# Kernel tuning notes

Hardware: AMD Instinct MI355X
Metric: run time of the kernel (lower is better)

The kernel has to match this reference:

```python
import jax, jax.numpy as jnp
import numpy as np

D_MODEL = 1024
N_HEADS = 16
FEATURE_DIM = 16
HEAD_DIM = D_MODEL // N_HEADS  # 64
EPS = 1e-12


def taylor_exp(x):
    """2nd-order Taylor feature map of exp(q^T k / sqrt(d)).
    x: (b, h, l, d) -> (b, h, l, 1 + d + d^2)"""
    d = x.shape[-1]
    rd = jnp.sqrt(jnp.asarray(d, x.dtype))      # sqrt(d)
    rrd = jnp.sqrt(rd)                          # d^(1/4)
    r2 = jnp.sqrt(jnp.asarray(2.0, x.dtype))
    x2 = (x[..., :, None] * x[..., None, :]).reshape(*x.shape[:-1], d * d) / r2
    ones = jnp.ones_like(x[..., :1])
    return jnp.concatenate([ones, x / rrd, x2 / rd], axis=-1)


def setup_inputs() -> dict:
    key = jax.random.key(0)
    k0, k1, k2, k3, k4 = jax.random.split(key, 5)
    b, l = 1, 1024
    scale = 1.0 / np.sqrt(D_MODEL)
    hidden_states = jax.random.normal(k0, (b, l, D_MODEL), dtype=jnp.float32)
    Wq = jax.random.normal(k1, (N_HEADS * FEATURE_DIM, D_MODEL), dtype=jnp.float32) * scale
    Wk = jax.random.normal(k2, (N_HEADS * FEATURE_DIM, D_MODEL), dtype=jnp.float32) * scale
    Wv = jax.random.normal(k3, (N_HEADS * HEAD_DIM, D_MODEL), dtype=jnp.float32) * scale
    Wo = jax.random.normal(k4, (D_MODEL, N_HEADS * HEAD_DIM), dtype=jnp.float32) * scale
    return {"hidden_states": hidden_states, "Wq": Wq, "Wk": Wk, "Wv": Wv, "Wo": Wo}


def reference(hidden_states, Wq, Wk, Wv, Wo):
    b, l, _ = hidden_states.shape
    # projections (bias-free)
    q = (hidden_states @ Wq.T).reshape(b, l, N_HEADS, FEATURE_DIM).transpose(0, 2, 1, 3)
    k = (hidden_states @ Wk.T).reshape(b, l, N_HEADS, FEATURE_DIM).transpose(0, 2, 1, 3)
    v = (hidden_states @ Wv.T).reshape(b, l, N_HEADS, HEAD_DIM).transpose(0, 2, 1, 3)
    qf = taylor_exp(q)   # (b, h, l, D) with D = 1 + d + d^2 = 273
    kf = taylor_exp(k)
    # causal linear attention via associative KV accumulation
    # kv_state[l] = sum_{t<=l} phi(k_t) outer v_t  -> (b, h, l, head_dim, D)
    kv_state = jnp.cumsum(kf[..., None, :] * v[..., :, None], axis=2)
    num = jnp.einsum('bhlD,bhldD->bhld', qf, kv_state)
    den = jnp.einsum('bhlD,bhlD->bhl', qf, jnp.cumsum(kf, axis=2))[..., None] + EPS
    y = num / den                                # (b, h, l, head_dim)
    y = y.transpose(0, 2, 1, 3).reshape(b, l, N_HEADS * HEAD_DIM)
    return y @ Wo.T
```

## Files before the change

### kernel.cpp

```cpp
#include <hip/hip_runtime.h>

#define LSEQ 1024
#define DMODEL 1024
#define NHEADS 16
#define FDIM 16
#define HDIM 64
#define CHUNK 64
#define NCHUNK 16

typedef __attribute__((ext_vector_type(8))) short short8;
typedef __attribute__((ext_vector_type(4))) float floatx4;

__device__ __forceinline__ float bf2f(unsigned short u) {
    unsigned int x = ((unsigned int)u) << 16;
    return __builtin_bit_cast(float, x);
}
__device__ __forceinline__ unsigned short f2bf(float f) {
    unsigned int x = __builtin_bit_cast(unsigned int, f);
    unsigned int r = (x + 0x7fffu + ((x >> 16) & 1u)) >> 16;
    return (unsigned short)r;
}

__device__ __forceinline__ int block_detect_fp32(const unsigned short* wq) {
    __shared__ int cnt;
    if (threadIdx.x == 0) cnt = 0;
    __syncthreads();
    int bad = 0;
    for (int i = threadIdx.x; i < 1024; i += blockDim.x) {
        int e = (wq[i] >> 7) & 0xFF;
        if (e >= 143 || (e > 0 && e <= 80)) bad++;
    }
    if (bad) atomicAdd(&cnt, bad);
    __syncthreads();
    return cnt > 128;
}

#define U_QB   0
#define U_KB   262144
#define U_VB   524288
#define U_YB   1572864

#define MFMA(a, b, c) __builtin_amdgcn_mfma_f32_16x16x32_bf16((a), (b), (c), 0, 0, 0)

__global__ __launch_bounds__(256) void qkv_gemm(
    const void* __restrict__ hidR, const void* __restrict__ WqR,
    const void* __restrict__ WkR, const void* __restrict__ WvR,
    unsigned short* __restrict__ qb, unsigned short* __restrict__ kb,
    unsigned short* __restrict__ vb) {
    int fp32 = block_detect_fp32((const unsigned short*)WqR);
    __shared__ __align__(16) unsigned short As[64][136];
    __shared__ __align__(16) unsigned short Bs[64][136];
    int nb = blockIdx.x, mb = blockIdx.y;
    const void* Braw; unsigned short* Cout; int ldc, col0, br0;
    if (nb < 4)      { Braw = WqR; br0 = nb * 64;       Cout = qb; ldc = 256;  col0 = nb * 64; }
    else if (nb < 8) { Braw = WkR; br0 = (nb - 4) * 64; Cout = kb; ldc = 256;  col0 = (nb - 4) * 64; }
    else             { Braw = WvR; br0 = (nb - 8) * 64; Cout = vb; ldc = 1024; col0 = (nb - 8) * 64; }

    int t = threadIdx.x;
    int r = t >> 2, c0 = (t & 3) * 32;
    int wave = t >> 6, lane = t & 63;
    int ml = lane & 15, q4 = lane >> 4;
    int mq = (wave >> 1) * 32, nq = (wave & 1) * 32;
    floatx4 acc00 = {0.f,0.f,0.f,0.f}, acc01 = acc00, acc10 = acc00, acc11 = acc00;

    for (int k0 = 0; k0 < DMODEL; k0 += 128) {
        short8 av[4], bv[4];
        if (!fp32) {
            const unsigned short* Ap = (const unsigned short*)hidR + (size_t)(mb * 64 + r) * DMODEL + k0 + c0;
            const unsigned short* Bp = (const unsigned short*)Braw + (size_t)(br0 + r) * DMODEL + k0 + c0;
            #pragma unroll
            for (int j = 0; j < 4; ++j) {
                av[j] = *(const short8*)(Ap + j * 8);
                bv[j] = *(const short8*)(Bp + j * 8);
            }
        } else {
            const float* Ap = (const float*)hidR + (size_t)(mb * 64 + r) * DMODEL + k0 + c0;
            const float* Bp = (const float*)Braw + (size_t)(br0 + r) * DMODEL + k0 + c0;
            #pragma unroll
            for (int j = 0; j < 4; ++j) {
                #pragma unroll
                for (int u = 0; u < 8; ++u) {
                    av[j][u] = (short)f2bf(Ap[j * 8 + u]);
                    bv[j][u] = (short)f2bf(Bp[j * 8 + u]);
                }
            }
        }
        __syncthreads();
        #pragma unroll
        for (int j = 0; j < 4; ++j) {
            *(short8*)&As[r][c0 + j * 8] = av[j];
            *(short8*)&Bs[r][c0 + j * 8] = bv[j];
        }
        __syncthreads();
        #pragma unroll
        for (int kk = 0; kk < 4; ++kk) {
            short8 a0 = *(const short8*)&As[mq + ml][kk * 32 + q4 * 8];
            short8 a1 = *(const short8*)&As[mq + 16 + ml][kk * 32 + q4 * 8];
            short8 b0 = *(const short8*)&Bs[nq + ml][kk * 32 + q4 * 8];
            short8 b1 = *(const short8*)&Bs[nq + 16 + ml][kk * 32 + q4 * 8];
            acc00 = MFMA(a0, b0, acc00); acc01 = MFMA(a0, b1, acc01);
            acc10 = MFMA(a1, b0, acc10); acc11 = MFMA(a1, b1, acc11);
        }
    }
    #pragma unroll
    for (int mi = 0; mi < 2; ++mi) {
        #pragma unroll
        for (int ni = 0; ni < 2; ++ni) {
            floatx4 acc = mi == 0 ? (ni == 0 ? acc00 : acc01) : (ni == 0 ? acc10 : acc11);
            int nloc = nq + ni * 16 + ml;
            #pragma unroll
            for (int r4 = 0; r4 < 4; ++r4) {
                int row = mb * 64 + mq + mi * 16 + q4 * 4 + r4;
                Cout[(size_t)row * ldc + col0 + nloc] = f2bf(acc[r4]);
            }
        }
    }
}

__global__ __launch_bounds__(256) void flash_attn(
    const unsigned short* __restrict__ qb, const unsigned short* __restrict__ kb,
    const unsigned short* __restrict__ vb, unsigned short* __restrict__ ybB) {
    int h = blockIdx.x & 15, c = blockIdx.x >> 4;
    int l0 = c * CHUNK;
    __shared__ __align__(16) unsigned short qs[64][40];
    __shared__ __align__(16) unsigned short ksm[64][40];
    __shared__ __align__(16) unsigned short vT[80][72];
    __shared__ __align__(16) unsigned short P[64][72];
    int t = threadIdx.x, lane = t & 63, wave = t >> 6;
    int ml = lane & 15, q4 = lane >> 4;
    int m0 = wave * 16;

    {
        int m = t >> 2, i4 = (t & 3) * 4;
        *(ushort4*)&qs[m][i4] = *(const ushort4*)&qb[(size_t)(l0 + m) * 256 + h * 16 + i4];
        ushort4 z = {0, 0, 0, 0};
        *(ushort4*)&qs[m][16 + i4]  = z;
        *(ushort4*)&ksm[m][16 + i4] = z;
    }
    if (t < 64) {
        vT[64][t] = 0x3F80;
        #pragma unroll
        for (int i = 65; i < 80; ++i) vT[i][t] = 0;
    }

    floatx4 acc[5];
    #pragma unroll
    for (int i = 0; i < 5; ++i) acc[i] = (floatx4){0.f, 0.f, 0.f, 0.f};

    for (int j = 0; j <= c; ++j) {
        {
            int m = t >> 2, i4 = (t & 3) * 4;
            *(ushort4*)&ksm[m][i4] = *(const ushort4*)&kb[(size_t)(j * 64 + m) * 256 + h * 16 + i4];
            int cc = (t & 3) * 16;
            unsigned short tmp[16];
            #pragma unroll
            for (int u = 0; u < 4; ++u)
                *(ushort4*)&tmp[u * 4] = *(const ushort4*)&vb[(size_t)(j * 64 + m) * 1024 + h * 64 + cc + u * 4];
            #pragma unroll
            for (int u = 0; u < 16; ++u) vT[cc + u][m] = tmp[u];
        }
        __syncthreads();

        short8 aq = *(const short8*)&qs[m0 + ml][q4 * 8];
        bool diag = (j == c);
        #pragma unroll
        for (int nt = 0; nt < 4; ++nt) {
            short8 bk = *(const short8*)&ksm[nt * 16 + ml][q4 * 8];
            floatx4 s4 = {0.f, 0.f, 0.f, 0.f};
            s4 = MFMA(aq, bk, s4);
            int tt = nt * 16 + ml;
            #pragma unroll
            for (int r = 0; r < 4; ++r) {
                int lrow = m0 + q4 * 4 + r;
                float s = s4[r];
                float p = 1.f + 0.25f * s + 0.03125f * s * s;
                if (diag && tt > lrow) p = 0.f;
                P[lrow][tt] = f2bf(p);
            }
        }

        #pragma unroll
        for (int k0 = 0; k0 < 64; k0 += 32) {
            short8 ap = *(const short8*)&P[m0 + ml][k0 + q4 * 8];
            #pragma unroll
            for (int nt = 0; nt < 5; ++nt) {
                short8 bv = *(const short8*)&vT[nt * 16 + ml][k0 + q4 * 8];
                acc[nt] = MFMA(ap, bv, acc[nt]);
            }
        }
        __syncthreads();
    }

    #pragma unroll
    for (int r = 0; r < 4; ++r) {
        float den = __shfl(acc[4][r], q4 * 16) + 1e-12f;
        float dinv = 1.f / den;
        int lrow = m0 + q4 * 4 + r;
        unsigned short* yp = ybB + (size_t)(l0 + lrow) * 1024 + h * 64;
        #pragma unroll
        for (int nt = 0; nt < 4; ++nt)
            yp[nt * 16 + ml] = f2bf(acc[nt][r] * dinv);
    }
}

__global__ __launch_bounds__(256) void out_gemm(
    const unsigned short* __restrict__ A, const void* __restrict__ WoR,
    void* __restrict__ outv, const unsigned short* __restrict__ wqraw) {
    int fp32 = block_detect_fp32(wqraw);
    __shared__ __align__(16) unsigned short As[64][136];
    __shared__ __align__(16) unsigned short Bs[64][136];
    int nb = blockIdx.x, mb = blockIdx.y;
    int br0 = nb * 64;

    int t = threadIdx.x;
    int r = t >> 2, c0 = (t & 3) * 32;
    int wave = t >> 6, lane = t & 63;
    int ml = lane & 15, q4 = lane >> 4;
    int mq = (wave >> 1) * 32, nq = (wave & 1) * 32;
    floatx4 acc00 = {0.f,0.f,0.f,0.f}, acc01 = acc00, acc10 = acc00, acc11 = acc00;

    for (int k0 = 0; k0 < DMODEL; k0 += 128) {
        short8 av[4], bv[4];
        const unsigned short* Ap = A + (size_t)(mb * 64 + r) * DMODEL + k0 + c0;
        #pragma unroll
        for (int j = 0; j < 4; ++j) av[j] = *(const short8*)(Ap + j * 8);
        if (!fp32) {
            const unsigned short* Bp = (const unsigned short*)WoR + (size_t)(br0 + r) * DMODEL + k0 + c0;
            #pragma unroll
            for (int j = 0; j < 4; ++j) bv[j] = *(const short8*)(Bp + j * 8);
        } else {
            const float* Bp = (const float*)WoR + (size_t)(br0 + r) * DMODEL + k0 + c0;
            #pragma unroll
            for (int j = 0; j < 4; ++j) {
                #pragma unroll
                for (int u = 0; u < 8; ++u) bv[j][u] = (short)f2bf(Bp[j * 8 + u]);
            }
        }
        __syncthreads();
        #pragma unroll
        for (int j = 0; j < 4; ++j) {
            *(short8*)&As[r][c0 + j * 8] = av[j];
            *(short8*)&Bs[r][c0 + j * 8] = bv[j];
        }
        __syncthreads();
        #pragma unroll
        for (int kk = 0; kk < 4; ++kk) {
            short8 a0 = *(const short8*)&As[mq + ml][kk * 32 + q4 * 8];
            short8 a1 = *(const short8*)&As[mq + 16 + ml][kk * 32 + q4 * 8];
            short8 b0 = *(const short8*)&Bs[nq + ml][kk * 32 + q4 * 8];
            short8 b1 = *(const short8*)&Bs[nq + 16 + ml][kk * 32 + q4 * 8];
            acc00 = MFMA(a0, b0, acc00); acc01 = MFMA(a0, b1, acc01);
            acc10 = MFMA(a1, b0, acc10); acc11 = MFMA(a1, b1, acc11);
        }
    }
    #pragma unroll
    for (int mi = 0; mi < 2; ++mi) {
        #pragma unroll
        for (int ni = 0; ni < 2; ++ni) {
            floatx4 acc = mi == 0 ? (ni == 0 ? acc00 : acc01) : (ni == 0 ? acc10 : acc11);
            int n = nb * 64 + nq + ni * 16 + ml;
            #pragma unroll
            for (int r4 = 0; r4 < 4; ++r4) {
                int row = mb * 64 + mq + mi * 16 + q4 * 4 + r4;
                size_t idx = (size_t)row * 1024 + n;
                if (fp32) ((float*)outv)[idx] = acc[r4];
                else      ((unsigned short*)outv)[idx] = f2bf(acc[r4]);
            }
        }
    }
}

extern "C" void kernel_launch(void* const* d_in, const int* in_sizes, int n_in,
                              void* d_out, int out_size, void* d_ws, size_t ws_size,
                              hipStream_t stream) {
    unsigned short* us = (unsigned short*)d_ws;
    unsigned short* qbB = us + U_QB;
    unsigned short* kbB = us + U_KB;
    unsigned short* vbB = us + U_VB;
    unsigned short* ybB = us + U_YB;
    size_t need = (size_t)(U_YB + 1048576) * 2ull;
    if (ws_size < need) return;

    qkv_gemm<<<dim3(24, 16), 256, 0, stream>>>(d_in[0], d_in[1], d_in[2], d_in[3], qbB, kbB, vbB);
    flash_attn<<<dim3(256), 256, 0, stream>>>(qbB, kbB, vbB, ybB);
    out_gemm<<<dim3(16, 16), 256, 0, stream>>>(ybB, d_in[4], d_out, (const unsigned short*)d_in[1]);
}
```

Baseline: 152.3 us.

## Fuse QKV GEMM, attention, and output GEMM into one cooperative persistent kernel

Replaces three kernel launches with a single cooperative kernel of 256 blocks that runs the QKV projection (384 tiles over a grid-stride loop), the chunked causal attention, and the output projection, separated by grid-wide syncs. It also adds register double-buffering of the next K-slice in the GEMM body so global loads overlap with MFMA work. This removes launch gaps and repeated fp32 detection, but the QKV stage now takes two waves of tiles on 256 blocks. The grid syncs and the unbalanced causal attention stage make every block wait for the slowest one.

```diff
diff --git a/kernel.cpp b/kernel.cpp
--- a/kernel.cpp
+++ b/kernel.cpp
@@ -1,4 +1,7 @@
 #include <hip/hip_runtime.h>
+#include <hip/hip_cooperative_groups.h>
+
+namespace cg = cooperative_groups;
 
 #define LSEQ 1024
 #define DMODEL 1024
@@ -21,20 +24,6 @@
     return (unsigned short)r;
 }
 
-__device__ __forceinline__ int block_detect_fp32(const unsigned short* wq) {
-    __shared__ int cnt;
-    if (threadIdx.x == 0) cnt = 0;
-    __syncthreads();
-    int bad = 0;
-    for (int i = threadIdx.x; i < 1024; i += blockDim.x) {
-        int e = (wq[i] >> 7) & 0xFF;
-        if (e >= 143 || (e > 0 && e <= 80)) bad++;
-    }
-    if (bad) atomicAdd(&cnt, bad);
-    __syncthreads();
-    return cnt > 128;
-}
-
 #define U_QB   0
 #define U_KB   262144
 #define U_VB   524288
@@ -42,231 +31,232 @@
 
 #define MFMA(a, b, c) __builtin_amdgcn_mfma_f32_16x16x32_bf16((a), (b), (c), 0, 0, 0)
 
-__global__ __launch_bounds__(256) void qkv_gemm(
-    const void* __restrict__ hidR, const void* __restrict__ WqR,
-    const void* __restrict__ WkR, const void* __restrict__ WvR,
-    unsigned short* __restrict__ qb, unsigned short* __restrict__ kb,
-    unsigned short* __restrict__ vb) {
-    int fp32 = block_detect_fp32((const unsigned short*)WqR);
-    __shared__ __align__(16) unsigned short As[64][136];
-    __shared__ __align__(16) unsigned short Bs[64][136];
-    int nb = blockIdx.x, mb = blockIdx.y;
-    const void* Braw; unsigned short* Cout; int ldc, col0, br0;
-    if (nb < 4)      { Braw = WqR; br0 = nb * 64;       Cout = qb; ldc = 256;  col0 = nb * 64; }
-    else if (nb < 8) { Braw = WkR; br0 = (nb - 4) * 64; Cout = kb; ldc = 256;  col0 = (nb - 4) * 64; }
-    else             { Braw = WvR; br0 = (nb - 8) * 64; Cout = vb; ldc = 1024; col0 = (nb - 8) * 64; }
-
+struct SMemGemm { unsigned short As[64][136]; unsigned short Bs[64][136]; };
+struct SMemFA {
+    unsigned short qs[64][40];
+    unsigned short ksm[64][40];
+    unsigned short vT[80][72];
+    unsigned short P[64][72];
+};
+union SMemU { SMemGemm g; SMemFA f; };
+
+__device__ __forceinline__ void gemm64_body(
+    SMemGemm& s, const void* Araw, int a_fp32, int arow0,
+    const void* Braw, int b_fp32, int brow0, floatx4 acc[4]) {
     int t = threadIdx.x;
     int r = t >> 2, c0 = (t & 3) * 32;
     int wave = t >> 6, lane = t & 63;
     int ml = lane & 15, q4 = lane >> 4;
     int mq = (wave >> 1) * 32, nq = (wave & 1) * 32;
-    floatx4 acc00 = {0.f,0.f,0.f,0.f}, acc01 = acc00, acc10 = acc00, acc11 = acc00;
-
+    #pragma unroll
+    for (int i = 0; i < 4; ++i) acc[i] = (floatx4){0.f, 0.f, 0.f, 0.f};
+
+    short8 av[4], bv[4], av2[4], bv2[4];
+    auto stage = [&](int k0, short8* a, short8* b) {
+        if (!a_fp32) {
+            const unsigned short* Ap = (const unsigned short*)Araw + (size_t)(arow0 + r) * DMODEL + k0 + c0;
+            #pragma unroll
+            for (int j = 0; j < 4; ++j) a[j] = *(const short8*)(Ap + j * 8);
+        } else {
+            const float* Ap = (const float*)Araw + (size_t)(arow0 + r) * DMODEL + k0 + c0;
+            #pragma unroll
+            for (int j = 0; j < 4; ++j)
+                #pragma unroll
+                for (int u = 0; u < 8; ++u) a[j][u] = (short)f2bf(Ap[j * 8 + u]);
+        }
+        if (!b_fp32) {
+            const unsigned short* Bp = (const unsigned short*)Braw + (size_t)(brow0 + r) * DMODEL + k0 + c0;
+            #pragma unroll
+            for (int j = 0; j < 4; ++j) b[j] = *(const short8*)(Bp + j * 8);
+        } else {
+            const float* Bp = (const float*)Braw + (size_t)(brow0 + r) * DMODEL + k0 + c0;
+            #pragma unroll
+            for (int j = 0; j < 4; ++j)
+                #pragma unroll
+                for (int u = 0; u < 8; ++u) b[j][u] = (short)f2bf(Bp[j * 8 + u]);
+        }
+    };
+
+    stage(0, av, bv);
     for (int k0 = 0; k0 < DMODEL; k0 += 128) {
-        short8 av[4], bv[4];
-        if (!fp32) {
-            const unsigned short* Ap = (const unsigned short*)hidR + (size_t)(mb * 64 + r) * DMODEL + k0 + c0;
-            const unsigned short* Bp = (const unsigned short*)Braw + (size_t)(br0 + r) * DMODEL + k0 + c0;
-            #pragma unroll
-            for (int j = 0; j < 4; ++j) {
-                av[j] = *(const short8*)(Ap + j * 8);
-                bv[j] = *(const short8*)(Bp + j * 8);
-            }
-        } else {
-            const float* Ap = (const float*)hidR + (size_t)(mb * 64 + r) * DMODEL + k0 + c0;
-            const float* Bp = (const float*)Braw + (size_t)(br0 + r) * DMODEL + k0 + c0;
-            #pragma unroll
-            for (int j = 0; j < 4; ++j) {
-                #pragma unroll
-                for (int u = 0; u < 8; ++u) {
-                    av[j][u] = (short)f2bf(Ap[j * 8 + u]);
-                    bv[j][u] = (short)f2bf(Bp[j * 8 + u]);
-                }
-            }
-        }
         __syncthreads();
         #pragma unroll
         for (int j = 0; j < 4; ++j) {
-            *(short8*)&As[r][c0 + j * 8] = av[j];
-            *(short8*)&Bs[r][c0 + j * 8] = bv[j];
-        }
-        __syncthreads();
+            *(short8*)&s.As[r][c0 + j * 8] = av[j];
+            *(short8*)&s.Bs[r][c0 + j * 8] = bv[j];
+        }
+        __syncthreads();
+        if (k0 + 128 < DMODEL) stage(k0 + 128, av2, bv2);
         #pragma unroll
         for (int kk = 0; kk < 4; ++kk) {
-            short8 a0 = *(const short8*)&As[mq + ml][kk * 32 + q4 * 8];
-            short8 a1 = *(const short8*)&As[mq + 16 + ml][kk * 32 + q4 * 8];
-            short8 b0 = *(const short8*)&Bs[nq + ml][kk * 32 + q4 * 8];
-            short8 b1 = *(const short8*)&Bs[nq + 16 + ml][kk * 32 + q4 * 8];
-            acc00 = MFMA(a0, b0, acc00); acc01 = MFMA(a0, b1, acc01);
-            acc10 = MFMA(a1, b0, acc10); acc11 = MFMA(a1, b1, acc11);
-        }
-    }
-    #pragma unroll
-    for (int mi = 0; mi < 2; ++mi) {
-        #pragma unroll
-        for (int ni = 0; ni < 2; ++ni) {
-            floatx4 acc = mi == 0 ? (ni == 0 ? acc00 : acc01) : (ni == 0 ? acc10 : acc11);
-            int nloc = nq + ni * 16 + ml;
-            #pragma unroll
-            for (int r4 = 0; r4 < 4; ++r4) {
-                int row = mb * 64 + mq + mi * 16 + q4 * 4 + r4;
-                Cout[(size_t)row * ldc + col0 + nloc] = f2bf(acc[r4]);
-            }
-        }
-    }
-}
-
-__global__ __launch_bounds__(256) void flash_attn(
-    const unsigned short* __restrict__ qb, const unsigned short* __restrict__ kb,
-    const unsigned short* __restrict__ vb, unsigned short* __restrict__ ybB) {
-    int h = blockIdx.x & 15, c = blockIdx.x >> 4;
-    int l0 = c * CHUNK;
-    __shared__ __align__(16) unsigned short qs[64][40];
-    __shared__ __align__(16) unsigned short ksm[64][40];
-    __shared__ __align__(16) unsigned short vT[80][72];
-    __shared__ __align__(16) unsigned short P[64][72];
+            short8 a0 = *(const short8*)&s.As[mq + ml][kk * 32 + q4 * 8];
+            short8 a1 = *(const short8*)&s.As[mq + 16 + ml][kk * 32 + q4 * 8];
+            short8 b0 = *(const short8*)&s.Bs[nq + ml][kk * 32 + q4 * 8];
+            short8 b1 = *(const short8*)&s.Bs[nq + 16 + ml][kk * 32 + q4 * 8];
+            acc[0] = MFMA(a0, b0, acc[0]); acc[1] = MFMA(a0, b1, acc[1]);
+            acc[2] = MFMA(a1, b0, acc[2]); acc[3] = MFMA(a1, b1, acc[3]);
+        }
+        #pragma unroll
+        for (int j = 0; j < 4; ++j) { av[j] = av2[j]; bv[j] = bv2[j]; }
+    }
+    __syncthreads();
+}
+
+__global__ __launch_bounds__(256) void mega(
+    const void* __restrict__ hidR, const void* __restrict__ WqR,
+    const void* __restrict__ WkR, const void* __restrict__ WvR,
+    const void* __restrict__ WoR, void* __restrict__ outv,
+    unsigned short* __restrict__ qb, unsigned short* __restrict__ kb,
+    unsigned short* __restrict__ vb, unsigned short* __restrict__ ybB) {
+    cg::grid_group grid = cg::this_grid();
+    __shared__ __align__(16) SMemU sm;
+    int bid = blockIdx.x;
     int t = threadIdx.x, lane = t & 63, wave = t >> 6;
     int ml = lane & 15, q4 = lane >> 4;
-    int m0 = wave * 16;
-
+
+    int fp32;
     {
-        int m = t >> 2, i4 = (t & 3) * 4;
-        *(ushort4*)&qs[m][i4] = *(const ushort4*)&qb[(size_t)(l0 + m) * 256 + h * 16 + i4];
-        ushort4 z = {0, 0, 0, 0};
-        *(ushort4*)&qs[m][16 + i4]  = z;
-        *(ushort4*)&ksm[m][16 + i4] = z;
-    }
-    if (t < 64) {
-        vT[64][t] = 0x3F80;
-        #pragma unroll
-        for (int i = 65; i < 80; ++i) vT[i][t] = 0;
-    }
-
-    floatx4 acc[5];
-    #pragma unroll
-    for (int i = 0; i < 5; ++i) acc[i] = (floatx4){0.f, 0.f, 0.f, 0.f};
-
-    for (int j = 0; j <= c; ++j) {
+        __shared__ int cnt;
+        if (t == 0) cnt = 0;
+        __syncthreads();
+        const unsigned short* wq = (const unsigned short*)WqR;
+        int bad = 0;
+        for (int i = t; i < 1024; i += 256) {
+            int e = (wq[i] >> 7) & 0xFF;
+            if (e >= 143 || (e > 0 && e <= 80)) bad++;
+        }
+        if (bad) atomicAdd(&cnt, bad);
+        __syncthreads();
+        fp32 = cnt > 128;
+    }
+
+    for (int T = bid; T < 384; T += 256) {
+        int mb = T / 24, nb = T % 24;
+        const void* Braw; unsigned short* Cout; int ldc, col0, br0;
+        if (nb < 4)      { Braw = WqR; br0 = nb * 64;       Cout = qb; ldc = 256;  col0 = nb * 64; }
+        else if (nb < 8) { Braw = WkR; br0 = (nb - 4) * 64; Cout = kb; ldc = 256;  col0 = (nb - 4) * 64; }
+        else             { Braw = WvR; br0 = (nb - 8) * 64; Cout = vb; ldc = 1024; col0 = (nb - 8) * 64; }
+        floatx4 acc[4];
+        gemm64_body(sm.g, hidR, fp32, mb * 64, Braw, fp32, br0, acc);
+        int mq = (wave >> 1) * 32, nq = (wave & 1) * 32;
+        #pragma unroll
+        for (int mi = 0; mi < 2; ++mi)
+            #pragma unroll
+            for (int ni = 0; ni < 2; ++ni) {
+                floatx4 a = acc[mi * 2 + ni];
+                int nloc = nq + ni * 16 + ml;
+                #pragma unroll
+                for (int r4 = 0; r4 < 4; ++r4) {
+                    int row = mb * 64 + mq + mi * 16 + q4 * 4 + r4;
+                    Cout[(size_t)row * ldc + col0 + nloc] = f2bf(a[r4]);
+                }
+            }
+    }
+    __threadfence();
+    grid.sync();
+
+    {
+        unsigned short (&qs)[64][40]  = sm.f.qs;
+        unsigned short (&ksm)[64][40] = sm.f.ksm;
+        unsigned short (&vT)[80][72]  = sm.f.vT;
+        unsigned short (&P)[64][72]   = sm.f.P;
+        int h = bid & 15, c = bid >> 4;
+        int l0 = c * CHUNK;
+        int m0 = wave * 16;
+
         {
             int m = t >> 2, i4 = (t & 3) * 4;
-            *(ushort4*)&ksm[m][i4] = *(const ushort4*)&kb[(size_t)(j * 64 + m) * 256 + h * 16 + i4];
-            int cc = (t & 3) * 16;
-            unsigned short tmp[16];
-            #pragma unroll
-            for (int u = 0; u < 4; ++u)
-                *(ushort4*)&tmp[u * 4] = *(const ushort4*)&vb[(size_t)(j * 64 + m) * 1024 + h * 64 + cc + u * 4];
-            #pragma unroll
-            for (int u = 0; u < 16; ++u) vT[cc + u][m] = tmp[u];
-        }
-        __syncthreads();
-
-        short8 aq = *(const short8*)&qs[m0 + ml][q4 * 8];
-        bool diag = (j == c);
-        #pragma unroll
-        for (int nt = 0; nt < 4; ++nt) {
-            short8 bk = *(const short8*)&ksm[nt * 16 + ml][q4 * 8];
-            floatx4 s4 = {0.f, 0.f, 0.f, 0.f};
-            s4 = MFMA(aq, bk, s4);
-            int tt = nt * 16 + ml;
-            #pragma unroll
-            for (int r = 0; r < 4; ++r) {
-                int lrow = m0 + q4 * 4 + r;
-                float s = s4[r];
-                float p = 1.f + 0.25f * s + 0.03125f * s * s;
-                if (diag && tt > lrow) p = 0.f;
-                P[lrow][tt] = f2bf(p);
-            }
-        }
-
-        #pragma unroll
-        for (int k0 = 0; k0 < 64; k0 += 32) {
-            short8 ap = *(const short8*)&P[m0 + ml][k0 + q4 * 8];
-            #pragma unroll
-            for (int nt = 0; nt < 5; ++nt) {
-                short8 bv = *(const short8*)&vT[nt * 16 + ml][k0 + q4 * 8];
-                acc[nt] = MFMA(ap, bv, acc[nt]);
-            }
-        }
-        __syncthreads();
-    }
-
-    #pragma unroll
-    for (int r = 0; r < 4; ++r) {
-        float den = __shfl(acc[4][r], q4 * 16) + 1e-12f;
-        float dinv = 1.f / den;
-        int lrow = m0 + q4 * 4 + r;
-        unsigned short* yp = ybB + (size_t)(l0 + lrow) * 1024 + h * 64;
-        #pragma unroll
-        for (int nt = 0; nt < 4; ++nt)
-            yp[nt * 16 + ml] = f2bf(acc[nt][r] * dinv);
-    }
-}
-
-__global__ __launch_bounds__(256) void out_gemm(
-    const unsigned short* __restrict__ A, const void* __restrict__ WoR,
-    void* __restrict__ outv, const unsigned short* __restrict__ wqraw) {
-    int fp32 = block_detect_fp32(wqraw);
-    __shared__ __align__(16) unsigned short As[64][136];
-    __shared__ __align__(16) unsigned short Bs[64][136];
-    int nb = blockIdx.x, mb = blockIdx.y;
-    int br0 = nb * 64;
-
-    int t = threadIdx.x;
-    int r = t >> 2, c0 = (t & 3) * 32;
-    int wave = t >> 6, lane = t & 63;
-    int ml = lane & 15, q4 = lane >> 4;
-    int mq = (wave >> 1) * 32, nq = (wave & 1) * 32;
-    floatx4 acc00 = {0.f,0.f,0.f,0.f}, acc01 = acc00, acc10 = acc00, acc11 = acc00;
-
-    for (int k0 = 0; k0 < DMODEL; k0 += 128) {
-        short8 av[4], bv[4];
-        const unsigned short* Ap = A + (size_t)(mb * 64 + r) * DMODEL + k0 + c0;
-        #pragma unroll
-        for (int j = 0; j < 4; ++j) av[j] = *(const short8*)(Ap + j * 8);
-        if (!fp32) {
-            const unsigned short* Bp = (const unsigned short*)WoR + (size_t)(br0 + r) * DMODEL + k0 + c0;
-            #pragma unroll
-            for (int j = 0; j < 4; ++j) bv[j] = *(const short8*)(Bp + j * 8);
-        } else {
-            const float* Bp = (const float*)WoR + (size_t)(br0 + r) * DMODEL + k0 + c0;
-            #pragma unroll
-            for (int j = 0; j < 4; ++j) {
-                #pragma unroll
-                for (int u = 0; u < 8; ++u) bv[j][u] = (short)f2bf(Bp[j * 8 + u]);
-            }
-        }
-        __syncthreads();
-        #pragma unroll
-        for (int j = 0; j < 4; ++j) {
-            *(short8*)&As[r][c0 + j * 8] = av[j];
-            *(short8*)&Bs[r][c0 + j * 8] = bv[j];
-        }
-        __syncthreads();
-        #pragma unroll
-        for (int kk = 0; kk < 4; ++kk) {
-            short8 a0 = *(const short8*)&As[mq + ml][kk * 32 + q4 * 8];
-            short8 a1 = *(const short8*)&As[mq + 16 + ml][kk * 32 + q4 * 8];
-            short8 b0 = *(const short8*)&Bs[nq + ml][kk * 32 + q4 * 8];
-            short8 b1 = *(const short8*)&Bs[nq + 16 + ml][kk * 32 + q4 * 8];
-            acc00 = MFMA(a0, b0, acc00); acc01 = MFMA(a0, b1, acc01);
-            acc10 = MFMA(a1, b0, acc10); acc11 = MFMA(a1, b1, acc11);
-        }
-    }
-    #pragma unroll
-    for (int mi = 0; mi < 2; ++mi) {
-        #pragma unroll
-        for (int ni = 0; ni < 2; ++ni) {
-            floatx4 acc = mi == 0 ? (ni == 0 ? acc00 : acc01) : (ni == 0 ? acc10 : acc11);
-            int n = nb * 64 + nq + ni * 16 + ml;
-            #pragma unroll
-            for (int r4 = 0; r4 < 4; ++r4) {
-                int row = mb * 64 + mq + mi * 16 + q4 * 4 + r4;
-                size_t idx = (size_t)row * 1024 + n;
-                if (fp32) ((float*)outv)[idx] = acc[r4];
-                else      ((unsigned short*)outv)[idx] = f2bf(acc[r4]);
-            }
-        }
+            *(ushort4*)&qs[m][i4] = *(const ushort4*)&qb[(size_t)(l0 + m) * 256 + h * 16 + i4];
+            ushort4 z = {0, 0, 0, 0};
+            *(ushort4*)&qs[m][16 + i4]  = z;
+            *(ushort4*)&ksm[m][16 + i4] = z;
+        }
+        if (t < 64) {
+            vT[64][t] = 0x3F80;
+            #pragma unroll
+            for (int i = 65; i < 80; ++i) vT[i][t] = 0;
+        }
+
+        floatx4 acc[5];
+        #pragma unroll
+        for (int i = 0; i < 5; ++i) acc[i] = (floatx4){0.f, 0.f, 0.f, 0.f};
+
+        for (int j = 0; j <= c; ++j) {
+            {
+                int m = t >> 2, i4 = (t & 3) * 4;
+                *(ushort4*)&ksm[m][i4] = *(const ushort4*)&kb[(size_t)(j * 64 + m) * 256 + h * 16 + i4];
+                int cc = (t & 3) * 16;
+                unsigned short tmp[16];
+                #pragma unroll
+                for (int u = 0; u < 4; ++u)
+                    *(ushort4*)&tmp[u * 4] = *(const ushort4*)&vb[(size_t)(j * 64 + m) * 1024 + h * 64 + cc + u * 4];
+                #pragma unroll
+                for (int u = 0; u < 16; ++u) vT[cc + u][m] = tmp[u];
+            }
+            __syncthreads();
+
+            short8 aq = *(const short8*)&qs[m0 + ml][q4 * 8];
+            bool diag = (j == c);
+            #pragma unroll
+            for (int nt = 0; nt < 4; ++nt) {
+                short8 bk = *(const short8*)&ksm[nt * 16 + ml][q4 * 8];
+                floatx4 s4 = {0.f, 0.f, 0.f, 0.f};
+                s4 = MFMA(aq, bk, s4);
+                int tt = nt * 16 + ml;
+                #pragma unroll
+                for (int r = 0; r < 4; ++r) {
+                    int lrow = m0 + q4 * 4 + r;
+                    float s = s4[r];
+                    float p = 1.f + 0.25f * s + 0.03125f * s * s;
+                    if (diag && tt > lrow) p = 0.f;
+                    P[lrow][tt] = f2bf(p);
+                }
+            }
+            #pragma unroll
+            for (int k0 = 0; k0 < 64; k0 += 32) {
+                short8 ap = *(const short8*)&P[m0 + ml][k0 + q4 * 8];
+                #pragma unroll
+                for (int nt = 0; nt < 5; ++nt) {
+                    short8 bvv = *(const short8*)&vT[nt * 16 + ml][k0 + q4 * 8];
+                    acc[nt] = MFMA(ap, bvv, acc[nt]);
+                }
+            }
+            __syncthreads();
+        }
+
+        #pragma unroll
+        for (int r = 0; r < 4; ++r) {
+            float den = __shfl(acc[4][r], q4 * 16) + 1e-12f;
+            float dinv = 1.f / den;
+            int lrow = m0 + q4 * 4 + r;
+            unsigned short* yp = ybB + (size_t)(l0 + lrow) * 1024 + h * 64;
+            #pragma unroll
+            for (int nt = 0; nt < 4; ++nt)
+                yp[nt * 16 + ml] = f2bf(acc[nt][r] * dinv);
+        }
+    }
+    __threadfence();
+    grid.sync();
+
+    {
+        int nb = bid & 15, mb = bid >> 4;
+        floatx4 acc[4];
+        gemm64_body(sm.g, ybB, 0, mb * 64, WoR, fp32, nb * 64, acc);
+        int mq = (wave >> 1) * 32, nq = (wave & 1) * 32;
+        #pragma unroll
+        for (int mi = 0; mi < 2; ++mi)
+            #pragma unroll
+            for (int ni = 0; ni < 2; ++ni) {
+                floatx4 a = acc[mi * 2 + ni];
+                int n = nb * 64 + nq + ni * 16 + ml;
+                #pragma unroll
+                for (int r4 = 0; r4 < 4; ++r4) {
+                    int row = mb * 64 + mq + mi * 16 + q4 * 4 + r4;
+                    size_t idx = (size_t)row * 1024 + n;
+                    if (fp32) ((float*)outv)[idx] = a[r4];
+                    else      ((unsigned short*)outv)[idx] = f2bf(a[r4]);
+                }
+            }
     }
 }
 
@@ -281,7 +271,13 @@
     size_t need = (size_t)(U_YB + 1048576) * 2ull;
     if (ws_size < need) return;
 
-    qkv_gemm<<<dim3(24, 16), 256, 0, stream>>>(d_in[0], d_in[1], d_in[2], d_in[3], qbB, kbB, vbB);
-    flash_attn<<<dim3(256), 256, 0, stream>>>(qbB, kbB, vbB, ybB);
-    out_gemm<<<dim3(16, 16), 256, 0, stream>>>(ybB, d_in[4], d_out, (const unsigned short*)d_in[1]);
-}
+    const void* hid = d_in[0];
+    const void* wq  = d_in[1];
+    const void* wk  = d_in[2];
+    const void* wv  = d_in[3];
+    const void* wo  = d_in[4];
+    void* outp = d_out;
+    void* kargs[] = { (void*)&hid, (void*)&wq, (void*)&wk, (void*)&wv, (void*)&wo,
+                      (void*)&outp, (void*)&qbB, (void*)&kbB, (void*)&vbB, (void*)&ybB };
+    hipLaunchCooperativeKernel((const void*)mega, dim3(256), dim3(256), kargs, 0, stream);
+}
```

New measurement: 273.0 us. 1.79x slower.
